# Kernel optimization log

Measured on AMD Instinct MI355X. Metric: run time of the kernel, lower is better.

Reference implementation:

```python
import jax, jax.numpy as jnp
import numpy as np

ALPHA = 0.001
TAU = 1.0
KAPPA = 1.0
N_ITER = 1


def setup_inputs() -> dict:
    key = jax.random.key(0)
    k1, k2, k3, k4, k5 = jax.random.split(key, 5)
    B, H, N, K = 8, 8, 512, 16
    mu = jax.random.normal(k1, (B, N, K), dtype=jnp.float32)
    # beta: softmax-like attention weights over j (positive, rows sum to 1)
    beta = jax.nn.softmax(jax.random.normal(k2, (B, H, N, N), dtype=jnp.float32), axis=-1)
    mu_prior = jax.random.normal(k3, (B, N, K), dtype=jnp.float32)
    phi = 0.1 * jax.random.normal(k4, (B, N, 3), dtype=jnp.float32)
    g = jax.random.normal(k5, (3, K, K), dtype=jnp.float32)
    generators = 0.5 * (g - jnp.swapaxes(g, -1, -2))  # skew-symmetric so(3) rep -> stable expm
    lr = jnp.asarray(0.05, dtype=jnp.float32)
    return {"mu": mu, "beta": beta, "mu_prior": mu_prior, "phi": phi,
            "generators": generators, "lr": lr}


def _transport(mu, phi, generators):
    # phi_algebra[b,n] = sum_g phi[b,n,g] * G_g  -> (B,N,K,K)
    B, N, K = mu.shape
    phi_alg = jnp.einsum('bng,gkl->bnkl', phi, generators)
    expm = jax.vmap(jax.scipy.linalg.expm)
    Om_i = expm(phi_alg.reshape(B * N, K, K)).reshape(B, N, K, K)
    Om_j_inv = expm((-phi_alg).reshape(B * N, K, K)).reshape(B, N, K, K)
    # mu_t[b,i,j] = Om_i[b,i] @ (Om_j_inv[b,j] @ mu[b,j])  (factored, avoids (B,N,N,K,K))
    v = jnp.einsum('bjlm,bjm->bjl', Om_j_inv, mu)          # (B,N,K)
    mu_t = jnp.einsum('bikl,bjl->bijk', Om_i, v)           # (B,N,N,K)
    return mu_t


def reference(mu, beta, mu_prior, phi, generators, lr):
    beta_avg = beta.mean(axis=1)                           # (B,N,N)
    mu_cur = mu
    for _ in range(N_ITER):
        grad_prior = ALPHA * (mu_cur - mu_prior)
        mu_t = _transport(mu_cur, phi, generators)         # (B,N,N,K)
        delta = mu_cur[:, :, None, :] - mu_t               # (B,N,N,K)
        # TERM 1: sum_j (beta_ij/tau) * delta_ij
        grad1 = jnp.einsum('bij,bijk->bik', beta_avg, delta) / TAU
        # TERM 2 (second-order): sum_j sum_k (beta_ij/kappa)(delta_jk - beta_ik) KL_ij gkl_ik
        #   = (1/kappa)[ sum_j beta_ij KL_ij gkl_ij - (sum_j beta_ij KL_ij) * sum_k beta_ik gkl_ik ]
        kl = jnp.sum(delta * delta, axis=-1) / (2.0 * TAU)  # (B,N,N)
        gkl = delta / TAU                                   # (B,N,N,K)
        w = beta_avg * kl                                   # (B,N,N)
        term1 = jnp.einsum('bij,bijk->bik', w, gkl)
        s = jnp.sum(w, axis=-1)                             # (B,N)
        bsum = jnp.einsum('bij,bijk->bik', beta_avg, gkl)
        grad2 = (term1 - s[..., None] * bsum) / KAPPA
        mu_cur = mu_cur - lr * (grad_prior + grad1 + grad2)
    return mu_cur
```

## Files before the change

kernel.cpp:

```cpp
#include <hip/hip_runtime.h>
#include <hip/hip_bf16.h>
#include <cstddef>
#include <cstdint>

#define B_ 8
#define H_ 8
#define N_ 512
#define K_ 16
#define NN_ (N_*N_)

static constexpr float ALPHA_C = 0.001f;

typedef float f32x4 __attribute__((ext_vector_type(4)));

#define LDSTRIDE 20

__device__ __forceinline__ void mm_rowB(const float* a, const float* Bbuf,
                                        int c0, f32x4& acc)
{
    #pragma unroll
    for (int k = 0; k < 16; ++k) {
        const f32x4 bk = *(const f32x4*)&Bbuf[k * LDSTRIDE + c0];
        acc.x = fmaf(a[k], bk.x, acc.x);
        acc.y = fmaf(a[k], bk.y, acc.y);
        acc.z = fmaf(a[k], bk.z, acc.z);
        acc.w = fmaf(a[k], bk.w, acc.w);
    }
}

__device__ __forceinline__ void read_row(const float* buf, int r, float* a)
{
    #pragma unroll
    for (int i = 0; i < 4; ++i) {
        const f32x4 t = *(const f32x4*)&buf[r * LDSTRIDE + 4 * i];
        a[4*i]   = t.x; a[4*i+1] = t.y; a[4*i+2] = t.z; a[4*i+3] = t.w;
    }
}

__device__ __forceinline__ void write_strip(float* buf, int r, int c0, f32x4 s)
{
    *(f32x4*)&buf[r * LDSTRIDE + c0] = s;
}

__global__ __launch_bounds__(256) void expm_kernel(
    const float* __restrict__ mu, const float* __restrict__ phi,
    const float* __restrict__ gen, float* __restrict__ Om,
    float* __restrict__ v, float* __restrict__ q)
{
    __shared__ float lds[4][2][16 * LDSTRIDE];

    const int tid  = threadIdx.x;
    const int w    = tid >> 6, lane = tid & 63;
    const int r    = lane >> 2, c0 = (lane & 3) << 2;
    const int bn   = (blockIdx.x << 2) | w;

    float* U0 = lds[w][0];
    float* U1 = lds[w][1];

    const float p0 = phi[bn*3+0], p1 = phi[bn*3+1], p2 = phi[bn*3+2];
    const int gidx = r * 16 + c0;
    const f32x4 g0 = *(const f32x4*)&gen[gidx];
    const f32x4 g1 = *(const f32x4*)&gen[256 + gidx];
    const f32x4 g2 = *(const f32x4*)&gen[512 + gidx];
    f32x4 As;
    As.x = p0*g0.x + p1*g1.x + p2*g2.x;
    As.y = p0*g0.y + p1*g1.y + p2*g2.y;
    As.z = p0*g0.z + p1*g1.z + p2*g2.z;
    As.w = p0*g0.w + p1*g1.w + p2*g2.w;

    float t = As.x*As.x + As.y*As.y + As.z*As.z + As.w*As.w;
    #pragma unroll
    for (int m = 1; m <= 32; m <<= 1) t += __shfl_xor(t, m, 64);
    float theta = sqrtf(t);
    int s = 0;
    while (theta > 2.0f && s < 30) { theta *= 0.5f; ++s; }
    const float sc = exp2f((float)(-s));
    const f32x4 Xs = As * sc;

    write_strip(U0, r, c0, Xs);
    float xrow[16];
    read_row(U0, r, xrow);

    f32x4 a2s = {0.f, 0.f, 0.f, 0.f};
    mm_rowB(xrow, U0, c0, a2s);
    write_strip(U1, r, c0, a2s);

    f32x4 a3s = {0.f, 0.f, 0.f, 0.f};
    mm_rowB(xrow, U1, c0, a3s);

    float a2row[16];
    read_row(U1, r, a2row);
    f32x4 a4s = {0.f, 0.f, 0.f, 0.f};
    mm_rowB(a2row, U1, c0, a4s);
    write_strip(U0, r, c0, a4s);
    float a4row[16];
    read_row(U0, r, a4row);

    f32x4 di = {0.f, 0.f, 0.f, 0.f};
    if (r >= c0 && r < c0 + 4) ((float*)&di)[r - c0] = 1.0f;

    const f32x4 C0 = di + Xs + a2s * 0.5f + a3s * (1.0f/6.0f);
    const f32x4 C1 = di * (1.0f/24.0f) + Xs * (1.0f/120.0f)
                   + a2s * (1.0f/720.0f) + a3s * (1.0f/5040.0f);
    const f32x4 Q2 = di * (1.0f/40320.0f) + Xs * (1.0f/362880.0f)
                   + a2s * (1.0f/3628800.0f) + a3s * (1.0f/39916800.0f)
                   + a4s * (1.0f/479001600.0f);

    write_strip(U1, r, c0, Q2);
    f32x4 T1 = C1;
    mm_rowB(a4row, U1, c0, T1);

    write_strip(U1, r, c0, T1);
    f32x4 P = C0;
    mm_rowB(a4row, U1, c0, P);

    for (int it = 0; it < s; ++it) {
        write_strip(U1, r, c0, P);
        float prow[16];
        read_row(U1, r, prow);
        f32x4 Pn = {0.f, 0.f, 0.f, 0.f};
        mm_rowB(prow, U1, c0, Pn);
        P = Pn;
    }

    *(f32x4*)&Om[(size_t)bn * 256 + r * 16 + c0] = P;

    const float mur = mu[bn * 16 + r];
    f32x4 vc = P * mur;
    #pragma unroll
    for (int m = 4; m <= 32; m <<= 1) {
        vc.x += __shfl_xor(vc.x, m, 64);
        vc.y += __shfl_xor(vc.y, m, 64);
        vc.z += __shfl_xor(vc.z, m, 64);
        vc.w += __shfl_xor(vc.w, m, 64);
    }
    if (r == 0) *(f32x4*)&v[bn * 16 + c0] = vc;

    float qp = vc.x*vc.x + vc.y*vc.y + vc.z*vc.z + vc.w*vc.w;
    qp += __shfl_xor(qp, 1, 64);
    qp += __shfl_xor(qp, 2, 64);
    if (lane == 0) q[bn] = 0.5f * qp;
}

__global__ __launch_bounds__(256, 4) void grad_kernel(
    const float* __restrict__ mu, const float* __restrict__ beta,
    const float* __restrict__ mu_prior, const float* __restrict__ lrp,
    const float* __restrict__ Om, const float* __restrict__ v,
    const float* __restrict__ q, float* __restrict__ out)
{
    __shared__ float v_t[16 * 516];
    __shared__ f32x4 q4[128];

    const int blk = blockIdx.x;
    const int b   = blk >> 7;
    const int i0  = (blk & 127) << 2;
    const int tid = threadIdx.x;
    const int wid = tid >> 6, lane = tid & 63;
    const int i   = i0 + wid;

    const float* vb = v + (size_t)b * N_ * K_;
    f32x4 tq[8];
    #pragma unroll
    for (int s = 0; s < 8; ++s)
        tq[s] = *(const f32x4*)&vb[(tid + 256 * s) << 2];

    f32x4 qreg = {0.f, 0.f, 0.f, 0.f};
    const f32x4* qb4 = (const f32x4*)(q + (size_t)b * N_);
    if (tid < 128) qreg = qb4[tid];

    const size_t betaBase = (((size_t)b * H_) * N_ + i) * N_;
    const float* bp = beta + betaBase + (lane << 2);
    f32x4 bt[16];
    #pragma unroll
    for (int h = 0; h < H_; ++h) {
        bt[2*h+0] = __builtin_nontemporal_load((const f32x4*)(bp + (size_t)h * NN_));
        bt[2*h+1] = __builtin_nontemporal_load((const f32x4*)(bp + (size_t)h * NN_ + 256));
    }

    #pragma unroll
    for (int s = 0; s < 8; ++s) {
        const int f4 = tid + 256 * s;
        const int j  = f4 >> 2;
        const int k0 = (f4 & 3) << 2;
        v_t[(k0+0) * 516 + j] = tq[s].x;
        v_t[(k0+1) * 516 + j] = tq[s].y;
        v_t[(k0+2) * 516 + j] = tq[s].z;
        v_t[(k0+3) * 516 + j] = tq[s].w;
    }
    if (tid < 128) q4[tid] = qreg;
    __syncthreads();

    f32x4 rv0 = bt[0], rv1 = bt[1];
    #pragma unroll
    for (int h = 1; h < H_; ++h) { rv0 += bt[2*h]; rv1 += bt[2*h+1]; }
    rv0 *= 0.125f; rv1 *= 0.125f;

    float vi[16];
    #pragma unroll
    for (int k = 0; k < 16; ++k) vi[k] = v_t[k * 516 + i];
    const float qi = ((const float*)q4)[i];

    float w1[16], w2[16];
    #pragma unroll
    for (int k = 0; k < 16; ++k) { w1[k] = 0.f; w2[k] = 0.f; }
    float sacc = 0.f, R = 0.f;

    #pragma unroll
    for (int p = 0; p < 2; ++p) {
        const int j0 = (lane << 2) | (p << 8);
        const float rx = p ? rv1.x : rv0.x;
        const float ry = p ? rv1.y : rv0.y;
        const float rz = p ? rv1.z : rv0.z;
        const float rw = p ? rv1.w : rv0.w;

        float d0 = 0.f, d1 = 0.f, d2 = 0.f, d3 = 0.f;
        #pragma unroll
        for (int k = 0; k < 16; ++k) {
            const f32x4 vj = *(const f32x4*)&v_t[k * 516 + j0];
            d0 = fmaf(vi[k], vj.x, d0);
            d1 = fmaf(vi[k], vj.y, d1);
            d2 = fmaf(vi[k], vj.z, d2);
            d3 = fmaf(vi[k], vj.w, d3);
        }
        const f32x4 qj = q4[lane | (p << 6)];
        const float rkl0 = rx * (qi + qj.x - d0);
        const float rkl1 = ry * (qi + qj.y - d1);
        const float rkl2 = rz * (qi + qj.z - d2);
        const float rkl3 = rw * (qi + qj.w - d3);
        sacc += (rkl0 + rkl1) + (rkl2 + rkl3);
        R    += (rx + ry) + (rz + rw);

        #pragma unroll
        for (int k = 0; k < 16; ++k) {
            const f32x4 vj = *(const f32x4*)&v_t[k * 516 + j0];
            float a1 = fmaf(rx, vj.x, w1[k]);
            a1 = fmaf(ry, vj.y, a1);
            a1 = fmaf(rz, vj.z, a1);
            w1[k] = fmaf(rw, vj.w, a1);
            float a2 = fmaf(rkl0, vj.x, w2[k]);
            a2 = fmaf(rkl1, vj.y, a2);
            a2 = fmaf(rkl2, vj.z, a2);
            w2[k] = fmaf(rkl3, vj.w, a2);
        }
    }

    #pragma unroll
    for (int off = 32; off > 0; off >>= 1) {
        sacc += __shfl_xor(sacc, off, 64);
        R    += __shfl_xor(R,    off, 64);
    }
    const float oms  = 1.0f - sacc;
    const float coef = oms * R + sacc;

    float wc[16];
    #pragma unroll
    for (int k = 0; k < 16; ++k) wc[k] = fmaf(oms, w1[k], w2[k]);

    {
        #pragma unroll
        for (int k = 0; k < 8; ++k) {
            const bool up = (lane & 32) != 0;
            const float send = up ? wc[k] : wc[k + 8];
            const float recv = __shfl_xor(send, 32, 64);
            wc[k] = (up ? wc[k + 8] : wc[k]) + recv;
        }
        #pragma unroll
        for (int k = 0; k < 4; ++k) {
            const bool up = (lane & 16) != 0;
            const float send = up ? wc[k] : wc[k + 4];
            const float recv = __shfl_xor(send, 16, 64);
            wc[k] = (up ? wc[k + 4] : wc[k]) + recv;
        }
        #pragma unroll
        for (int k = 0; k < 2; ++k) {
            const bool up = (lane & 8) != 0;
            const float send = up ? wc[k] : wc[k + 2];
            const float recv = __shfl_xor(send, 8, 64);
            wc[k] = (up ? wc[k + 2] : wc[k]) + recv;
        }
        {
            const bool up = (lane & 4) != 0;
            const float send = up ? wc[0] : wc[1];
            const float recv = __shfl_xor(send, 4, 64);
            wc[0] = (up ? wc[1] : wc[0]) + recv;
        }
        wc[0] += __shfl_xor(wc[0], 2, 64);
        wc[0] += __shfl_xor(wc[0], 1, 64);
    }

    const int cmine = (lane >> 2) & 15;
    const float gv = coef * v_t[cmine * 516 + i] - wc[0];

    const size_t rowi = (size_t)b * N_ + i;
    const float* omb = Om + rowi * 256;
    const int tqi = lane & 3;
    float pr[4];
    #pragma unroll
    for (int rr = 0; rr < 4; ++rr)
        pr[rr] = omb[(4 * tqi + rr) * 16 + cmine] * gv;

    #pragma unroll
    for (int k = 0; k < 2; ++k) {
        const bool up = (lane & 4) != 0;
        const float send = up ? pr[k] : pr[k + 2];
        const float recv = __shfl_xor(send, 4, 64);
        pr[k] = (up ? pr[k + 2] : pr[k]) + recv;
    }
    {
        const bool up = (lane & 8) != 0;
        const float send = up ? pr[0] : pr[1];
        const float recv = __shfl_xor(send, 8, 64);
        pr[0] = (up ? pr[1] : pr[0]) + recv;
    }
    pr[0] += __shfl_xor(pr[0], 16, 64);
    pr[0] += __shfl_xor(pr[0], 32, 64);

    if (lane < 16) {
        const int row = 4 * tqi + 2 * ((lane >> 2) & 1) + ((lane >> 3) & 1);
        const float lr = lrp[0];
        const size_t oi = rowi * 16 + row;
        const float m0 = mu[oi], mp = mu_prior[oi];
        out[oi] = m0 - lr * (ALPHA_C * (m0 - mp) + pr[0]);
    }
}

extern "C" void kernel_launch(void* const* d_in, const int* in_sizes, int n_in,
                              void* d_out, int out_size, void* d_ws, size_t ws_size,
                              hipStream_t stream)
{
    const float* mu   = (const float*)d_in[0];
    const float* beta = (const float*)d_in[1];
    const float* mup  = (const float*)d_in[2];
    const float* phi  = (const float*)d_in[3];
    const float* gen  = (const float*)d_in[4];
    const float* lr   = (const float*)d_in[5];
    float* out = (float*)d_out;

    float* Om = (float*)d_ws;
    float* v  = Om + (size_t)4096 * 256;
    float* q  = v  + (size_t)4096 * 16;

    expm_kernel<<<B_ * N_ / 4, 256, 0, stream>>>(mu, phi, gen, Om, v, q);
    grad_kernel<<<B_ * (N_ / 4), 256, 0, stream>>>(mu, beta, mup, lr, Om, v, q, out);
}
```

Baseline: 122.1 us.

## Move beta head-averaging into expm kernel to overlap loads with matrix exponential

Streaming and averaging the 8 beta heads moves out of the gradient kernel into the expm kernel, where the loads are issued in two batches interleaved with the Padé/squaring work so memory latency hides behind compute. The averaged beta goes to a new 8 MB workspace buffer that the gradient kernel reads back. The gradient kernel also hoists its Om, mu and mu_prior loads and unrolls the two j halves explicitly. This adds an extra write and read of the averaged matrix and more register pressure in the expm kernel under a 4-block launch bound.

Result: slower. 159.6 us (+30.7%).

```diff
diff --git a/kernel.cpp b/kernel.cpp
--- a/kernel.cpp
+++ b/kernel.cpp
@@ -42,10 +42,11 @@
     *(f32x4*)&buf[r * LDSTRIDE + c0] = s;
 }
 
-__global__ __launch_bounds__(256) void expm_kernel(
+__global__ __launch_bounds__(256, 4) void expm_beta_kernel(
     const float* __restrict__ mu, const float* __restrict__ phi,
-    const float* __restrict__ gen, float* __restrict__ Om,
-    float* __restrict__ v, float* __restrict__ q)
+    const float* __restrict__ gen, const float* __restrict__ beta,
+    float* __restrict__ Om, float* __restrict__ v, float* __restrict__ q,
+    float* __restrict__ bavg)
 {
     __shared__ float lds[4][2][16 * LDSTRIDE];
 
@@ -53,6 +54,8 @@
     const int w    = tid >> 6, lane = tid & 63;
     const int r    = lane >> 2, c0 = (lane & 3) << 2;
     const int bn   = (blockIdx.x << 2) | w;
+    const int bb   = bn >> 9;
+    const int nn   = bn & 511;
 
     float* U0 = lds[w][0];
     float* U1 = lds[w][1];
@@ -62,6 +65,17 @@
     const f32x4 g0 = *(const f32x4*)&gen[gidx];
     const f32x4 g1 = *(const f32x4*)&gen[256 + gidx];
     const f32x4 g2 = *(const f32x4*)&gen[512 + gidx];
+    const float mur = mu[bn * 16 + r];
+
+    const size_t betaBase = (((size_t)bb * H_) * N_ + nn) * N_;
+    const float* bp = beta + betaBase + (lane << 2);
+    f32x4 bt[8];
+    #pragma unroll
+    for (int h = 0; h < 4; ++h) {
+        bt[2*h+0] = __builtin_nontemporal_load((const f32x4*)(bp + (size_t)h * NN_));
+        bt[2*h+1] = __builtin_nontemporal_load((const f32x4*)(bp + (size_t)h * NN_ + 256));
+    }
+
     f32x4 As;
     As.x = p0*g0.x + p1*g1.x + p2*g2.x;
     As.y = p0*g0.y + p1*g1.y + p2*g2.y;
@@ -96,6 +110,14 @@
     float a4row[16];
     read_row(U0, r, a4row);
 
+    f32x4 rv0 = (bt[0] + bt[2]) + (bt[4] + bt[6]);
+    f32x4 rv1 = (bt[1] + bt[3]) + (bt[5] + bt[7]);
+    #pragma unroll
+    for (int h = 4; h < 8; ++h) {
+        bt[2*(h-4)+0] = __builtin_nontemporal_load((const f32x4*)(bp + (size_t)h * NN_));
+        bt[2*(h-4)+1] = __builtin_nontemporal_load((const f32x4*)(bp + (size_t)h * NN_ + 256));
+    }
+
     f32x4 di = {0.f, 0.f, 0.f, 0.f};
     if (r >= c0 && r < c0 + 4) ((float*)&di)[r - c0] = 1.0f;
 
@@ -125,7 +147,6 @@
 
     *(f32x4*)&Om[(size_t)bn * 256 + r * 16 + c0] = P;
 
-    const float mur = mu[bn * 16 + r];
     f32x4 vc = P * mur;
     #pragma unroll
     for (int m = 4; m <= 32; m <<= 1) {
@@ -140,13 +161,19 @@
     qp += __shfl_xor(qp, 1, 64);
     qp += __shfl_xor(qp, 2, 64);
     if (lane == 0) q[bn] = 0.5f * qp;
+
+    rv0 = (rv0 + (bt[0] + bt[2])) + (bt[4] + bt[6]);
+    rv1 = (rv1 + (bt[1] + bt[3])) + (bt[5] + bt[7]);
+    float* bo = bavg + (size_t)bn * N_ + (lane << 2);
+    *(f32x4*)bo         = rv0 * 0.125f;
+    *(f32x4*)(bo + 256) = rv1 * 0.125f;
 }
 
 __global__ __launch_bounds__(256, 4) void grad_kernel(
-    const float* __restrict__ mu, const float* __restrict__ beta,
-    const float* __restrict__ mu_prior, const float* __restrict__ lrp,
-    const float* __restrict__ Om, const float* __restrict__ v,
-    const float* __restrict__ q, float* __restrict__ out)
+    const float* __restrict__ mu, const float* __restrict__ mu_prior,
+    const float* __restrict__ lrp, const float* __restrict__ Om,
+    const float* __restrict__ v, const float* __restrict__ q,
+    const float* __restrict__ bavg, float* __restrict__ out)
 {
     __shared__ float v_t[16 * 516];
     __shared__ f32x4 q4[128];
@@ -157,6 +184,25 @@
     const int tid = threadIdx.x;
     const int wid = tid >> 6, lane = tid & 63;
     const int i   = i0 + wid;
+    const size_t rowi = (size_t)b * N_ + i;
+
+    const float* bpr = bavg + rowi * N_ + (lane << 2);
+    const f32x4 rv0 = *(const f32x4*)bpr;
+    const f32x4 rv1 = *(const f32x4*)(bpr + 256);
+
+    const int cmine = (lane >> 2) & 15;
+    const int tqi   = lane & 3;
+    const float* omb = Om + rowi * 256;
+    float omr[4];
+    #pragma unroll
+    for (int rr = 0; rr < 4; ++rr)
+        omr[rr] = omb[(4 * tqi + rr) * 16 + cmine];
+
+    const int row = 4 * tqi + 2 * ((lane >> 2) & 1) + ((lane >> 3) & 1);
+    const size_t oi = rowi * 16 + row;
+    float m0 = 0.f, mp = 0.f;
+    if (lane < 16) { m0 = mu[oi]; mp = mu_prior[oi]; }
+    const float lrv = lrp[0];
 
     const float* vb = v + (size_t)b * N_ * K_;
     f32x4 tq[8];
@@ -167,15 +213,6 @@
     f32x4 qreg = {0.f, 0.f, 0.f, 0.f};
     const f32x4* qb4 = (const f32x4*)(q + (size_t)b * N_);
     if (tid < 128) qreg = qb4[tid];
-
-    const size_t betaBase = (((size_t)b * H_) * N_ + i) * N_;
-    const float* bp = beta + betaBase + (lane << 2);
-    f32x4 bt[16];
-    #pragma unroll
-    for (int h = 0; h < H_; ++h) {
-        bt[2*h+0] = __builtin_nontemporal_load((const f32x4*)(bp + (size_t)h * NN_));
-        bt[2*h+1] = __builtin_nontemporal_load((const f32x4*)(bp + (size_t)h * NN_ + 256));
-    }
 
     #pragma unroll
     for (int s = 0; s < 8; ++s) {
@@ -190,58 +227,75 @@
     if (tid < 128) q4[tid] = qreg;
     __syncthreads();
 
-    f32x4 rv0 = bt[0], rv1 = bt[1];
-    #pragma unroll
-    for (int h = 1; h < H_; ++h) { rv0 += bt[2*h]; rv1 += bt[2*h+1]; }
-    rv0 *= 0.125f; rv1 *= 0.125f;
-
     float vi[16];
     #pragma unroll
     for (int k = 0; k < 16; ++k) vi[k] = v_t[k * 516 + i];
     const float qi = ((const float*)q4)[i];
 
+    const int j0 = lane << 2;
+
+    float dA0 = 0.f, dA1 = 0.f, dA2 = 0.f, dA3 = 0.f;
+    #pragma unroll
+    for (int k = 0; k < 16; ++k) {
+        const f32x4 vj = *(const f32x4*)&v_t[k * 516 + j0];
+        dA0 = fmaf(vi[k], vj.x, dA0);
+        dA1 = fmaf(vi[k], vj.y, dA1);
+        dA2 = fmaf(vi[k], vj.z, dA2);
+        dA3 = fmaf(vi[k], vj.w, dA3);
+    }
+    float dB0 = 0.f, dB1 = 0.f, dB2 = 0.f, dB3 = 0.f;
+    #pragma unroll
+    for (int k = 0; k < 16; ++k) {
+        const f32x4 vj = *(const f32x4*)&v_t[k * 516 + j0 + 256];
+        dB0 = fmaf(vi[k], vj.x, dB0);
+        dB1 = fmaf(vi[k], vj.y, dB1);
+        dB2 = fmaf(vi[k], vj.z, dB2);
+        dB3 = fmaf(vi[k], vj.w, dB3);
+    }
+
+    const f32x4 qjA = q4[lane];
+    const f32x4 qjB = q4[lane | 64];
+    const float rklA0 = rv0.x * (qi + qjA.x - dA0);
+    const float rklA1 = rv0.y * (qi + qjA.y - dA1);
+    const float rklA2 = rv0.z * (qi + qjA.z - dA2);
+    const float rklA3 = rv0.w * (qi + qjA.w - dA3);
+    const float rklB0 = rv1.x * (qi + qjB.x - dB0);
+    const float rklB1 = rv1.y * (qi + qjB.y - dB1);
+    const float rklB2 = rv1.z * (qi + qjB.z - dB2);
+    const float rklB3 = rv1.w * (qi + qjB.w - dB3);
+
+    float sacc = ((rklA0 + rklA1) + (rklA2 + rklA3))
+               + ((rklB0 + rklB1) + (rklB2 + rklB3));
+    float R    = ((rv0.x + rv0.y) + (rv0.z + rv0.w))
+               + ((rv1.x + rv1.y) + (rv1.z + rv1.w));
+
     float w1[16], w2[16];
     #pragma unroll
     for (int k = 0; k < 16; ++k) { w1[k] = 0.f; w2[k] = 0.f; }
-    float sacc = 0.f, R = 0.f;
-
-    #pragma unroll
-    for (int p = 0; p < 2; ++p) {
-        const int j0 = (lane << 2) | (p << 8);
-        const float rx = p ? rv1.x : rv0.x;
-        const float ry = p ? rv1.y : rv0.y;
-        const float rz = p ? rv1.z : rv0.z;
-        const float rw = p ? rv1.w : rv0.w;
-
-        float d0 = 0.f, d1 = 0.f, d2 = 0.f, d3 = 0.f;
-        #pragma unroll
-        for (int k = 0; k < 16; ++k) {
-            const f32x4 vj = *(const f32x4*)&v_t[k * 516 + j0];
-            d0 = fmaf(vi[k], vj.x, d0);
-            d1 = fmaf(vi[k], vj.y, d1);
-            d2 = fmaf(vi[k], vj.z, d2);
-            d3 = fmaf(vi[k], vj.w, d3);
-        }
-        const f32x4 qj = q4[lane | (p << 6)];
-        const float rkl0 = rx * (qi + qj.x - d0);
-        const float rkl1 = ry * (qi + qj.y - d1);
-        const float rkl2 = rz * (qi + qj.z - d2);
-        const float rkl3 = rw * (qi + qj.w - d3);
-        sacc += (rkl0 + rkl1) + (rkl2 + rkl3);
-        R    += (rx + ry) + (rz + rw);
-
-        #pragma unroll
-        for (int k = 0; k < 16; ++k) {
-            const f32x4 vj = *(const f32x4*)&v_t[k * 516 + j0];
-            float a1 = fmaf(rx, vj.x, w1[k]);
-            a1 = fmaf(ry, vj.y, a1);
-            a1 = fmaf(rz, vj.z, a1);
-            w1[k] = fmaf(rw, vj.w, a1);
-            float a2 = fmaf(rkl0, vj.x, w2[k]);
-            a2 = fmaf(rkl1, vj.y, a2);
-            a2 = fmaf(rkl2, vj.z, a2);
-            w2[k] = fmaf(rkl3, vj.w, a2);
-        }
+
+    #pragma unroll
+    for (int k = 0; k < 16; ++k) {
+        const f32x4 vj = *(const f32x4*)&v_t[k * 516 + j0];
+        float a1 = fmaf(rv0.x, vj.x, w1[k]);
+        a1 = fmaf(rv0.y, vj.y, a1);
+        a1 = fmaf(rv0.z, vj.z, a1);
+        w1[k] = fmaf(rv0.w, vj.w, a1);
+        float a2 = fmaf(rklA0, vj.x, w2[k]);
+        a2 = fmaf(rklA1, vj.y, a2);
+        a2 = fmaf(rklA2, vj.z, a2);
+        w2[k] = fmaf(rklA3, vj.w, a2);
+    }
+    #pragma unroll
+    for (int k = 0; k < 16; ++k) {
+        const f32x4 vj = *(const f32x4*)&v_t[k * 516 + j0 + 256];
+        float a1 = fmaf(rv1.x, vj.x, w1[k]);
+        a1 = fmaf(rv1.y, vj.y, a1);
+        a1 = fmaf(rv1.z, vj.z, a1);
+        w1[k] = fmaf(rv1.w, vj.w, a1);
+        float a2 = fmaf(rklB0, vj.x, w2[k]);
+        a2 = fmaf(rklB1, vj.y, a2);
+        a2 = fmaf(rklB2, vj.z, a2);
+        w2[k] = fmaf(rklB3, vj.w, a2);
     }
 
     #pragma unroll
@@ -288,16 +342,12 @@
         wc[0] += __shfl_xor(wc[0], 1, 64);
     }
 
-    const int cmine = (lane >> 2) & 15;
     const float gv = coef * v_t[cmine * 516 + i] - wc[0];
 
-    const size_t rowi = (size_t)b * N_ + i;
-    const float* omb = Om + rowi * 256;
-    const int tqi = lane & 3;
     float pr[4];
     #pragma unroll
     for (int rr = 0; rr < 4; ++rr)
-        pr[rr] = omb[(4 * tqi + rr) * 16 + cmine] * gv;
+        pr[rr] = omr[rr] * gv;
 
     #pragma unroll
     for (int k = 0; k < 2; ++k) {
@@ -316,11 +366,7 @@
     pr[0] += __shfl_xor(pr[0], 32, 64);
 
     if (lane < 16) {
-        const int row = 4 * tqi + 2 * ((lane >> 2) & 1) + ((lane >> 3) & 1);
-        const float lr = lrp[0];
-        const size_t oi = rowi * 16 + row;
-        const float m0 = mu[oi], mp = mu_prior[oi];
-        out[oi] = m0 - lr * (ALPHA_C * (m0 - mp) + pr[0]);
+        out[oi] = m0 - lrv * (ALPHA_C * (m0 - mp) + pr[0]);
     }
 }
 
@@ -336,10 +382,11 @@
     const float* lr   = (const float*)d_in[5];
     float* out = (float*)d_out;
 
-    float* Om = (float*)d_ws;
-    float* v  = Om + (size_t)4096 * 256;
-    float* q  = v  + (size_t)4096 * 16;
-
-    expm_kernel<<<B_ * N_ / 4, 256, 0, stream>>>(mu, phi, gen, Om, v, q);
-    grad_kernel<<<B_ * (N_ / 4), 256, 0, stream>>>(mu, beta, mup, lr, Om, v, q, out);
-}
+    float* Om   = (float*)d_ws;
+    float* v    = Om + (size_t)4096 * 256;
+    float* q    = v  + (size_t)4096 * 16;
+    float* bavg = q  + (size_t)4096;
+
+    expm_beta_kernel<<<B_ * N_ / 4, 256, 0, stream>>>(mu, phi, gen, beta, Om, v, q, bavg);
+    grad_kernel<<<B_ * (N_ / 4), 256, 0, stream>>>(mu, mup, lr, Om, v, q, bavg, out);
+}
```

## Process two rows per wave in grad kernel and prefetch second beta row

Applied to the files above, without the earlier changes.

Each block now handles 8 query rows instead of 4, with every wave computing two rows (ia, ib). The v_t tile staged in LDS and every LDS read of v_j are shared across both rows, and the second row's beta loads are issued after the first row's head-average so they overlap with the dot-product compute. This halves the per-row cost of the v transpose into LDS and of the LDS reads in the inner loops. In exchange register pressure rises (launch bounds lowered from 4 to 3 blocks per CU) and the grid has half as many blocks, which may reduce the latency hiding available for the bandwidth-bound beta stream.

Result: slower. 164.2 us (+34.5%).

```diff
diff --git a/kernel.cpp b/kernel.cpp
--- a/kernel.cpp
+++ b/kernel.cpp
@@ -142,7 +142,65 @@
     if (lane == 0) q[bn] = 0.5f * qp;
 }
 
-__global__ __launch_bounds__(256, 4) void grad_kernel(
+__device__ __forceinline__ float fold16(float* wc, int lane)
+{
+    #pragma unroll
+    for (int k = 0; k < 8; ++k) {
+        const bool up = (lane & 32) != 0;
+        const float send = up ? wc[k] : wc[k + 8];
+        const float recv = __shfl_xor(send, 32, 64);
+        wc[k] = (up ? wc[k + 8] : wc[k]) + recv;
+    }
+    #pragma unroll
+    for (int k = 0; k < 4; ++k) {
+        const bool up = (lane & 16) != 0;
+        const float send = up ? wc[k] : wc[k + 4];
+        const float recv = __shfl_xor(send, 16, 64);
+        wc[k] = (up ? wc[k + 4] : wc[k]) + recv;
+    }
+    #pragma unroll
+    for (int k = 0; k < 2; ++k) {
+        const bool up = (lane & 8) != 0;
+        const float send = up ? wc[k] : wc[k + 2];
+        const float recv = __shfl_xor(send, 8, 64);
+        wc[k] = (up ? wc[k + 2] : wc[k]) + recv;
+    }
+    {
+        const bool up = (lane & 4) != 0;
+        const float send = up ? wc[0] : wc[1];
+        const float recv = __shfl_xor(send, 4, 64);
+        wc[0] = (up ? wc[1] : wc[0]) + recv;
+    }
+    wc[0] += __shfl_xor(wc[0], 2, 64);
+    wc[0] += __shfl_xor(wc[0], 1, 64);
+    return wc[0];
+}
+
+__device__ __forceinline__ float rot_reduce(const float* omr, float gv, int lane)
+{
+    float pr[4];
+    #pragma unroll
+    for (int rr = 0; rr < 4; ++rr) pr[rr] = omr[rr] * gv;
+
+    #pragma unroll
+    for (int k = 0; k < 2; ++k) {
+        const bool up = (lane & 4) != 0;
+        const float send = up ? pr[k] : pr[k + 2];
+        const float recv = __shfl_xor(send, 4, 64);
+        pr[k] = (up ? pr[k + 2] : pr[k]) + recv;
+    }
+    {
+        const bool up = (lane & 8) != 0;
+        const float send = up ? pr[0] : pr[1];
+        const float recv = __shfl_xor(send, 8, 64);
+        pr[0] = (up ? pr[1] : pr[0]) + recv;
+    }
+    pr[0] += __shfl_xor(pr[0], 16, 64);
+    pr[0] += __shfl_xor(pr[0], 32, 64);
+    return pr[0];
+}
+
+__global__ __launch_bounds__(256, 3) void grad_kernel(
     const float* __restrict__ mu, const float* __restrict__ beta,
     const float* __restrict__ mu_prior, const float* __restrict__ lrp,
     const float* __restrict__ Om, const float* __restrict__ v,
@@ -152,11 +210,12 @@
     __shared__ f32x4 q4[128];
 
     const int blk = blockIdx.x;
-    const int b   = blk >> 7;
-    const int i0  = (blk & 127) << 2;
+    const int b   = blk >> 6;
+    const int i0  = (blk & 63) << 3;
     const int tid = threadIdx.x;
     const int wid = tid >> 6, lane = tid & 63;
-    const int i   = i0 + wid;
+    const int ia  = i0 + wid;
+    const int ib  = i0 + 4 + wid;
 
     const float* vb = v + (size_t)b * N_ * K_;
     f32x4 tq[8];
@@ -168,13 +227,12 @@
     const f32x4* qb4 = (const f32x4*)(q + (size_t)b * N_);
     if (tid < 128) qreg = qb4[tid];
 
-    const size_t betaBase = (((size_t)b * H_) * N_ + i) * N_;
-    const float* bp = beta + betaBase + (lane << 2);
+    const float* bpA = beta + (((size_t)b * H_) * N_ + ia) * N_ + (lane << 2);
     f32x4 bt[16];
     #pragma unroll
     for (int h = 0; h < H_; ++h) {
-        bt[2*h+0] = __builtin_nontemporal_load((const f32x4*)(bp + (size_t)h * NN_));
-        bt[2*h+1] = __builtin_nontemporal_load((const f32x4*)(bp + (size_t)h * NN_ + 256));
+        bt[2*h+0] = __builtin_nontemporal_load((const f32x4*)(bpA + (size_t)h * NN_));
+        bt[2*h+1] = __builtin_nontemporal_load((const f32x4*)(bpA + (size_t)h * NN_ + 256));
     }
 
     #pragma unroll
@@ -190,137 +248,184 @@
     if (tid < 128) q4[tid] = qreg;
     __syncthreads();
 
-    f32x4 rv0 = bt[0], rv1 = bt[1];
-    #pragma unroll
-    for (int h = 1; h < H_; ++h) { rv0 += bt[2*h]; rv1 += bt[2*h+1]; }
-    rv0 *= 0.125f; rv1 *= 0.125f;
-
-    float vi[16];
-    #pragma unroll
-    for (int k = 0; k < 16; ++k) vi[k] = v_t[k * 516 + i];
-    const float qi = ((const float*)q4)[i];
-
-    float w1[16], w2[16];
-    #pragma unroll
-    for (int k = 0; k < 16; ++k) { w1[k] = 0.f; w2[k] = 0.f; }
-    float sacc = 0.f, R = 0.f;
-
-    #pragma unroll
-    for (int p = 0; p < 2; ++p) {
-        const int j0 = (lane << 2) | (p << 8);
-        const float rx = p ? rv1.x : rv0.x;
-        const float ry = p ? rv1.y : rv0.y;
-        const float rz = p ? rv1.z : rv0.z;
-        const float rw = p ? rv1.w : rv0.w;
-
-        float d0 = 0.f, d1 = 0.f, d2 = 0.f, d3 = 0.f;
-        #pragma unroll
-        for (int k = 0; k < 16; ++k) {
-            const f32x4 vj = *(const f32x4*)&v_t[k * 516 + j0];
-            d0 = fmaf(vi[k], vj.x, d0);
-            d1 = fmaf(vi[k], vj.y, d1);
-            d2 = fmaf(vi[k], vj.z, d2);
-            d3 = fmaf(vi[k], vj.w, d3);
-        }
-        const f32x4 qj = q4[lane | (p << 6)];
-        const float rkl0 = rx * (qi + qj.x - d0);
-        const float rkl1 = ry * (qi + qj.y - d1);
-        const float rkl2 = rz * (qi + qj.z - d2);
-        const float rkl3 = rw * (qi + qj.w - d3);
-        sacc += (rkl0 + rkl1) + (rkl2 + rkl3);
-        R    += (rx + ry) + (rz + rw);
-
-        #pragma unroll
-        for (int k = 0; k < 16; ++k) {
-            const f32x4 vj = *(const f32x4*)&v_t[k * 516 + j0];
-            float a1 = fmaf(rx, vj.x, w1[k]);
-            a1 = fmaf(ry, vj.y, a1);
-            a1 = fmaf(rz, vj.z, a1);
-            w1[k] = fmaf(rw, vj.w, a1);
-            float a2 = fmaf(rkl0, vj.x, w2[k]);
-            a2 = fmaf(rkl1, vj.y, a2);
-            a2 = fmaf(rkl2, vj.z, a2);
-            w2[k] = fmaf(rkl3, vj.w, a2);
-        }
-    }
+    f32x4 rvA0 = (((bt[0]+bt[2]) + (bt[4]+bt[6]))
+                + ((bt[8]+bt[10]) + (bt[12]+bt[14]))) * 0.125f;
+    f32x4 rvA1 = (((bt[1]+bt[3]) + (bt[5]+bt[7]))
+                + ((bt[9]+bt[11]) + (bt[13]+bt[15]))) * 0.125f;
+
+    const float* bpB = beta + (((size_t)b * H_) * N_ + ib) * N_ + (lane << 2);
+    #pragma unroll
+    for (int h = 0; h < H_; ++h) {
+        bt[2*h+0] = __builtin_nontemporal_load((const f32x4*)(bpB + (size_t)h * NN_));
+        bt[2*h+1] = __builtin_nontemporal_load((const f32x4*)(bpB + (size_t)h * NN_ + 256));
+    }
+
+    float via[16], vib[16];
+    #pragma unroll
+    for (int k = 0; k < 16; ++k) { via[k] = v_t[k * 516 + ia]; vib[k] = v_t[k * 516 + ib]; }
+    const float qia = ((const float*)q4)[ia];
+    const float qib = ((const float*)q4)[ib];
+
+    const int j0 = lane << 2;
+
+    float dAa0=0.f,dAa1=0.f,dAa2=0.f,dAa3=0.f, dAb0=0.f,dAb1=0.f,dAb2=0.f,dAb3=0.f;
+    #pragma unroll
+    for (int k = 0; k < 16; ++k) {
+        const f32x4 vj = *(const f32x4*)&v_t[k * 516 + j0];
+        dAa0 = fmaf(via[k], vj.x, dAa0);
+        dAa1 = fmaf(via[k], vj.y, dAa1);
+        dAa2 = fmaf(via[k], vj.z, dAa2);
+        dAa3 = fmaf(via[k], vj.w, dAa3);
+        dAb0 = fmaf(vib[k], vj.x, dAb0);
+        dAb1 = fmaf(vib[k], vj.y, dAb1);
+        dAb2 = fmaf(vib[k], vj.z, dAb2);
+        dAb3 = fmaf(vib[k], vj.w, dAb3);
+    }
+    float dBa0=0.f,dBa1=0.f,dBa2=0.f,dBa3=0.f, dBb0=0.f,dBb1=0.f,dBb2=0.f,dBb3=0.f;
+    #pragma unroll
+    for (int k = 0; k < 16; ++k) {
+        const f32x4 vj = *(const f32x4*)&v_t[k * 516 + j0 + 256];
+        dBa0 = fmaf(via[k], vj.x, dBa0);
+        dBa1 = fmaf(via[k], vj.y, dBa1);
+        dBa2 = fmaf(via[k], vj.z, dBa2);
+        dBa3 = fmaf(via[k], vj.w, dBa3);
+        dBb0 = fmaf(vib[k], vj.x, dBb0);
+        dBb1 = fmaf(vib[k], vj.y, dBb1);
+        dBb2 = fmaf(vib[k], vj.z, dBb2);
+        dBb3 = fmaf(vib[k], vj.w, dBb3);
+    }
+
+    const f32x4 rvB0 = (((bt[0]+bt[2]) + (bt[4]+bt[6]))
+                      + ((bt[8]+bt[10]) + (bt[12]+bt[14]))) * 0.125f;
+    const f32x4 rvB1 = (((bt[1]+bt[3]) + (bt[5]+bt[7]))
+                      + ((bt[9]+bt[11]) + (bt[13]+bt[15]))) * 0.125f;
+
+    const f32x4 qjA = q4[lane];
+    const f32x4 qjB = q4[lane | 64];
+
+    const float rklAa0 = rvA0.x * (qia + qjA.x - dAa0);
+    const float rklAa1 = rvA0.y * (qia + qjA.y - dAa1);
+    const float rklAa2 = rvA0.z * (qia + qjA.z - dAa2);
+    const float rklAa3 = rvA0.w * (qia + qjA.w - dAa3);
+    const float rklBa0 = rvA1.x * (qia + qjB.x - dBa0);
+    const float rklBa1 = rvA1.y * (qia + qjB.y - dBa1);
+    const float rklBa2 = rvA1.z * (qia + qjB.z - dBa2);
+    const float rklBa3 = rvA1.w * (qia + qjB.w - dBa3);
+
+    const float rklAb0 = rvB0.x * (qib + qjA.x - dAb0);
+    const float rklAb1 = rvB0.y * (qib + qjA.y - dAb1);
+    const float rklAb2 = rvB0.z * (qib + qjA.z - dAb2);
+    const float rklAb3 = rvB0.w * (qib + qjA.w - dAb3);
+    const float rklBb0 = rvB1.x * (qib + qjB.x - dBb0);
+    const float rklBb1 = rvB1.y * (qib + qjB.y - dBb1);
+    const float rklBb2 = rvB1.z * (qib + qjB.z - dBb2);
+    const float rklBb3 = rvB1.w * (qib + qjB.w - dBb3);
+
+    float sacc_a = ((rklAa0 + rklAa1) + (rklAa2 + rklAa3))
+                 + ((rklBa0 + rklBa1) + (rklBa2 + rklBa3));
+    float sacc_b = ((rklAb0 + rklAb1) + (rklAb2 + rklAb3))
+                 + ((rklBb0 + rklBb1) + (rklBb2 + rklBb3));
+    float R_a = ((rvA0.x + rvA0.y) + (rvA0.z + rvA0.w))
+              + ((rvA1.x + rvA1.y) + (rvA1.z + rvA1.w));
+    float R_b = ((rvB0.x + rvB0.y) + (rvB0.z + rvB0.w))
+              + ((rvB1.x + rvB1.y) + (rvB1.z + rvB1.w));
+
+    float w1a[16], w2a[16], w1b[16], w2b[16];
+    #pragma unroll
+    for (int k = 0; k < 16; ++k) { w1a[k]=0.f; w2a[k]=0.f; w1b[k]=0.f; w2b[k]=0.f; }
+
+    #pragma unroll
+    for (int k = 0; k < 16; ++k) {
+        const f32x4 vj = *(const f32x4*)&v_t[k * 516 + j0];
+        float t1 = fmaf(rvA0.x, vj.x, w1a[k]);
+        t1 = fmaf(rvA0.y, vj.y, t1);
+        t1 = fmaf(rvA0.z, vj.z, t1);
+        w1a[k] = fmaf(rvA0.w, vj.w, t1);
+        float t2 = fmaf(rklAa0, vj.x, w2a[k]);
+        t2 = fmaf(rklAa1, vj.y, t2);
+        t2 = fmaf(rklAa2, vj.z, t2);
+        w2a[k] = fmaf(rklAa3, vj.w, t2);
+        float t3 = fmaf(rvB0.x, vj.x, w1b[k]);
+        t3 = fmaf(rvB0.y, vj.y, t3);
+        t3 = fmaf(rvB0.z, vj.z, t3);
+        w1b[k] = fmaf(rvB0.w, vj.w, t3);
+        float t4 = fmaf(rklAb0, vj.x, w2b[k]);
+        t4 = fmaf(rklAb1, vj.y, t4);
+        t4 = fmaf(rklAb2, vj.z, t4);
+        w2b[k] = fmaf(rklAb3, vj.w, t4);
+    }
+    #pragma unroll
+    for (int k = 0; k < 16; ++k) {
+        const f32x4 vj = *(const f32x4*)&v_t[k * 516 + j0 + 256];
+        float t1 = fmaf(rvA1.x, vj.x, w1a[k]);
+        t1 = fmaf(rvA1.y, vj.y, t1);
+        t1 = fmaf(rvA1.z, vj.z, t1);
+        w1a[k] = fmaf(rvA1.w, vj.w, t1);
+        float t2 = fmaf(rklBa0, vj.x, w2a[k]);
+        t2 = fmaf(rklBa1, vj.y, t2);
+        t2 = fmaf(rklBa2, vj.z, t2);
+        w2a[k] = fmaf(rklBa3, vj.w, t2);
+        float t3 = fmaf(rvB1.x, vj.x, w1b[k]);
+        t3 = fmaf(rvB1.y, vj.y, t3);
+        t3 = fmaf(rvB1.z, vj.z, t3);
+        w1b[k] = fmaf(rvB1.w, vj.w, t3);
+        float t4 = fmaf(rklBb0, vj.x, w2b[k]);
+        t4 = fmaf(rklBb1, vj.y, t4);
+        t4 = fmaf(rklBb2, vj.z, t4);
+        w2b[k] = fmaf(rklBb3, vj.w, t4);
+    }
+
+    const int cmine = (lane >> 2) & 15;
+    const int tqi   = lane & 3;
+    const size_t rowia = (size_t)b * N_ + ia;
+    const size_t rowib = (size_t)b * N_ + ib;
+    const float* omba = Om + rowia * 256;
+    const float* ombb = Om + rowib * 256;
+    float omra[4], omrb[4];
+    #pragma unroll
+    for (int rr = 0; rr < 4; ++rr) {
+        omra[rr] = omba[(4 * tqi + rr) * 16 + cmine];
+        omrb[rr] = ombb[(4 * tqi + rr) * 16 + cmine];
+    }
+    const int row = 4 * tqi + 2 * ((lane >> 2) & 1) + ((lane >> 3) & 1);
+    const size_t oia = rowia * 16 + row;
+    const size_t oib = rowib * 16 + row;
+    float m0a = 0.f, mpa = 0.f, m0b = 0.f, mpb = 0.f;
+    if (lane < 16) {
+        m0a = mu[oia]; mpa = mu_prior[oia];
+        m0b = mu[oib]; mpb = mu_prior[oib];
+    }
+    const float lrv = lrp[0];
 
     #pragma unroll
     for (int off = 32; off > 0; off >>= 1) {
-        sacc += __shfl_xor(sacc, off, 64);
-        R    += __shfl_xor(R,    off, 64);
-    }
-    const float oms  = 1.0f - sacc;
-    const float coef = oms * R + sacc;
-
-    float wc[16];
-    #pragma unroll
-    for (int k = 0; k < 16; ++k) wc[k] = fmaf(oms, w1[k], w2[k]);
-
-    {
-        #pragma unroll
-        for (int k = 0; k < 8; ++k) {
-            const bool up = (lane & 32) != 0;
-            const float send = up ? wc[k] : wc[k + 8];
-            const float recv = __shfl_xor(send, 32, 64);
-            wc[k] = (up ? wc[k + 8] : wc[k]) + recv;
-        }
-        #pragma unroll
-        for (int k = 0; k < 4; ++k) {
-            const bool up = (lane & 16) != 0;
-            const float send = up ? wc[k] : wc[k + 4];
-            const float recv = __shfl_xor(send, 16, 64);
-            wc[k] = (up ? wc[k + 4] : wc[k]) + recv;
-        }
-        #pragma unroll
-        for (int k = 0; k < 2; ++k) {
-            const bool up = (lane & 8) != 0;
-            const float send = up ? wc[k] : wc[k + 2];
-            const float recv = __shfl_xor(send, 8, 64);
-            wc[k] = (up ? wc[k + 2] : wc[k]) + recv;
-        }
-        {
-            const bool up = (lane & 4) != 0;
-            const float send = up ? wc[0] : wc[1];
-            const float recv = __shfl_xor(send, 4, 64);
-            wc[0] = (up ? wc[1] : wc[0]) + recv;
-        }
-        wc[0] += __shfl_xor(wc[0], 2, 64);
-        wc[0] += __shfl_xor(wc[0], 1, 64);
-    }
-
-    const int cmine = (lane >> 2) & 15;
-    const float gv = coef * v_t[cmine * 516 + i] - wc[0];
-
-    const size_t rowi = (size_t)b * N_ + i;
-    const float* omb = Om + rowi * 256;
-    const int tqi = lane & 3;
-    float pr[4];
-    #pragma unroll
-    for (int rr = 0; rr < 4; ++rr)
-        pr[rr] = omb[(4 * tqi + rr) * 16 + cmine] * gv;
-
-    #pragma unroll
-    for (int k = 0; k < 2; ++k) {
-        const bool up = (lane & 4) != 0;
-        const float send = up ? pr[k] : pr[k + 2];
-        const float recv = __shfl_xor(send, 4, 64);
-        pr[k] = (up ? pr[k + 2] : pr[k]) + recv;
-    }
-    {
-        const bool up = (lane & 8) != 0;
-        const float send = up ? pr[0] : pr[1];
-        const float recv = __shfl_xor(send, 8, 64);
-        pr[0] = (up ? pr[1] : pr[0]) + recv;
-    }
-    pr[0] += __shfl_xor(pr[0], 16, 64);
-    pr[0] += __shfl_xor(pr[0], 32, 64);
+        sacc_a += __shfl_xor(sacc_a, off, 64);
+        R_a    += __shfl_xor(R_a,    off, 64);
+        sacc_b += __shfl_xor(sacc_b, off, 64);
+        R_b    += __shfl_xor(R_b,    off, 64);
+    }
+    const float oms_a  = 1.0f - sacc_a;
+    const float coef_a = oms_a * R_a + sacc_a;
+    const float oms_b  = 1.0f - sacc_b;
+    const float coef_b = oms_b * R_b + sacc_b;
+
+    float wca[16], wcb[16];
+    #pragma unroll
+    for (int k = 0; k < 16; ++k) {
+        wca[k] = fmaf(oms_a, w1a[k], w2a[k]);
+        wcb[k] = fmaf(oms_b, w1b[k], w2b[k]);
+    }
+    const float wfa = fold16(wca, lane);
+    const float wfb = fold16(wcb, lane);
+
+    const float gva = coef_a * v_t[cmine * 516 + ia] - wfa;
+    const float gvb = coef_b * v_t[cmine * 516 + ib] - wfb;
+    const float pra = rot_reduce(omra, gva, lane);
+    const float prb = rot_reduce(omrb, gvb, lane);
 
     if (lane < 16) {
-        const int row = 4 * tqi + 2 * ((lane >> 2) & 1) + ((lane >> 3) & 1);
-        const float lr = lrp[0];
-        const size_t oi = rowi * 16 + row;
-        const float m0 = mu[oi], mp = mu_prior[oi];
-        out[oi] = m0 - lr * (ALPHA_C * (m0 - mp) + pr[0]);
+        out[oia] = m0a - lrv * (ALPHA_C * (m0a - mpa) + pra);
+        out[oib] = m0b - lrv * (ALPHA_C * (m0b - mpb) + prb);
     }
 }
 
@@ -341,5 +446,5 @@
     float* q  = v  + (size_t)4096 * 16;
 
     expm_kernel<<<B_ * N_ / 4, 256, 0, stream>>>(mu, phi, gen, Om, v, q);
-    grad_kernel<<<B_ * (N_ / 4), 256, 0, stream>>>(mu, beta, mup, lr, Om, v, q, out);
-}
+    grad_kernel<<<B_ * (N_ / 8), 256, 0, stream>>>(mu, beta, mup, lr, Om, v, q, out);
+}
```
